# Performance work log

Hardware: AMD Instinct MI355X
Metric: run time of the kernel (lower is better)

## Reference

```python
import jax, jax.numpy as jnp
import numpy as np
import math

NV, NC, NE = 25000, 12500, 250000
DV_LP = DC_LP = 16
D_IN = 128   # in_var_dim = in_con_dim = in_edge_dim
D_OUT = 128  # out_var_dim = out_con_dim = out_edge_dim
E_WO = 5
EDGE_IN = D_IN + 3 + E_WO       # 136 = num_edge_lp_f_with_ss(8) + in_edge_dim(128)
VAR_COMB = DV_LP + D_IN          # 144
CON_COMB = DC_LP + D_IN          # 144

def _lin(key, din, dout, bias=True):
    k1, k2 = jax.random.split(key)
    W = jax.random.normal(k1, (din, dout), jnp.float32) * 0.05
    if bias:
        return W, jax.random.normal(k2, (dout,), jnp.float32) * 0.05
    return W, None

def setup_inputs():
    key = jax.random.key(0)
    ks = iter(jax.random.split(key, 64))
    d = {}
    d["var_learned_f"] = jax.random.normal(next(ks), (NV, D_IN), jnp.float32)
    d["var_lp_f"] = jax.random.normal(next(ks), (NV, DV_LP), jnp.float32)
    d["con_learned_f"] = jax.random.normal(next(ks), (NC, D_IN), jnp.float32)
    d["con_lp_f"] = jax.random.normal(next(ks), (NC, DC_LP), jnp.float32)
    d["edge_learned_f"] = jax.random.normal(next(ks), (NE, D_IN), jnp.float32)
    d["lo_costs"] = jax.random.normal(next(ks), (NE,), jnp.float32)
    d["hi_costs"] = jax.random.normal(next(ks), (NE,), jnp.float32)
    d["def_mm"] = jax.random.normal(next(ks), (NE,), jnp.float32)
    d["edge_lp_f_wo_ss"] = jax.random.normal(next(ks), (NE, E_WO), jnp.float32)
    # con_updater TransformerConv: src=var_comb(144), dst=con_comb(144), edge(136) -> 128
    d["cu_Wq"], d["cu_bq"] = _lin(next(ks), CON_COMB, D_OUT)
    d["cu_Wk"], d["cu_bk"] = _lin(next(ks), VAR_COMB, D_OUT)
    d["cu_Wv"], d["cu_bv"] = _lin(next(ks), VAR_COMB, D_OUT)
    d["cu_We"], _ = _lin(next(ks), EDGE_IN, D_OUT, bias=False)
    d["cu_Ws"], d["cu_bs"] = _lin(next(ks), CON_COMB, D_OUT)
    # var_updater TransformerConv: src=new con_comb(144), dst=var_comb(144)
    d["vu_Wq"], d["vu_bq"] = _lin(next(ks), VAR_COMB, D_OUT)
    d["vu_Wk"], d["vu_bk"] = _lin(next(ks), CON_COMB, D_OUT)
    d["vu_Wv"], d["vu_bv"] = _lin(next(ks), CON_COMB, D_OUT)
    d["vu_We"], _ = _lin(next(ks), EDGE_IN, D_OUT, bias=False)
    d["vu_Ws"], d["vu_bs"] = _lin(next(ks), VAR_COMB, D_OUT)
    # EdgeUpdater MLPs (hidden = out_edge_dim = 128, num_hidden_layers_edge = 0)
    d["eu_vW1"], d["eu_vb1"] = _lin(next(ks), VAR_COMB, D_OUT)
    d["eu_vW2"], d["eu_vb2"] = _lin(next(ks), D_OUT, D_OUT)
    d["eu_cW1"], d["eu_cb1"] = _lin(next(ks), CON_COMB, D_OUT)
    d["eu_cW2"], d["eu_cb2"] = _lin(next(ks), D_OUT, D_OUT)
    d["eu_eW1"], d["eu_eb1"] = _lin(next(ks), EDGE_IN + 2 * D_OUT, D_OUT)
    d["eu_eW2"], d["eu_eb2"] = _lin(next(ks), D_OUT, D_OUT)
    d["edge_index_var"] = jax.random.randint(next(ks), (NE,), 0, NV)
    d["edge_index_con"] = jax.random.randint(next(ks), (NE,), 0, NC)
    return d

def transformer_conv(x_src, x_dst, src_idx, dst_idx, e,
                     Wq, bq, Wk, bk, Wv, bv, We, Ws, bs, n_dst):
    # PyG TransformerConv, heads=1, edge_dim, aggr='mean', root_weight=True
    C = Wq.shape[1]
    q = x_dst @ Wq + bq                      # [N_dst, C]
    k = x_src @ Wk + bk                      # [N_src, C]
    v = x_src @ Wv + bv
    ee = e @ We                              # [E, C] (lin_edge, no bias)
    kj = k[src_idx] + ee
    alpha = jnp.sum(q[dst_idx] * kj, axis=-1) * (1.0 / math.sqrt(C))  # [E]
    # segment softmax over destination nodes
    amax = jax.ops.segment_max(alpha, dst_idx, num_segments=n_dst)
    ex = jnp.exp(alpha - amax[dst_idx])
    denom = jax.ops.segment_sum(ex, dst_idx, num_segments=n_dst)
    a = ex / denom[dst_idx]
    msg = (v[src_idx] + ee) * a[:, None]
    agg = jax.ops.segment_sum(msg, dst_idx, num_segments=n_dst)
    cnt = jax.ops.segment_sum(jnp.ones_like(alpha), dst_idx, num_segments=n_dst)
    out = agg / jnp.maximum(cnt, 1.0)[:, None]   # aggr='mean'
    return out + x_dst @ Ws + bs                 # skip connection (lin_skip)

def _forward(var_learned_f, var_lp_f, con_learned_f, con_lp_f, edge_learned_f,
             lo_costs, hi_costs, def_mm, edge_lp_f_wo_ss,
             cu_Wq, cu_bq, cu_Wk, cu_bk, cu_Wv, cu_bv, cu_We, cu_Ws, cu_bs,
             vu_Wq, vu_bq, vu_Wk, vu_bk, vu_Wv, vu_bv, vu_We, vu_Ws, vu_bs,
             eu_vW1, eu_vb1, eu_vW2, eu_vb2, eu_cW1, eu_cb1, eu_cW2, eu_cb2,
             eu_eW1, eu_eb1, eu_eW2, eu_eb2,
             edge_index_var, edge_index_con):
    relu = jax.nn.relu
    var_comb = jnp.concatenate([var_learned_f, var_lp_f], axis=1)     # [NV,144]
    con_comb = jnp.concatenate([con_learned_f, con_lp_f], axis=1)     # [NC,144]
    edge_comb = jnp.concatenate([edge_learned_f, lo_costs[:, None], hi_costs[:, None],
                                 def_mm[:, None], edge_lp_f_wo_ss], axis=1)  # [NE,136]
    # con update: messages from vars (edge_index[0]) to cons (edge_index[1])
    con_new = relu(transformer_conv(var_comb, con_comb, edge_index_var, edge_index_con,
                                    edge_comb, cu_Wq, cu_bq, cu_Wk, cu_bk, cu_Wv, cu_bv,
                                    cu_We, cu_Ws, cu_bs, NC))
    con_comb = jnp.concatenate([con_new, con_lp_f], axis=1)
    # var update: flow target_to_source -> messages from cons (edge_index[1]) to vars (edge_index[0])
    var_new = relu(transformer_conv(con_comb, var_comb, edge_index_con, edge_index_var,
                                    edge_comb, vu_Wq, vu_bq, vu_Wk, vu_bk, vu_Wv, vu_bv,
                                    vu_We, vu_Ws, vu_bs, NV))
    var_comb = jnp.concatenate([var_new, var_lp_f], axis=1)
    # edge update: compress nodes, gather to edges, concat, MLP
    vc = relu(relu(var_comb @ eu_vW1 + eu_vb1) @ eu_vW2 + eu_vb2)     # [NV,128]
    cc = relu(relu(con_comb @ eu_cW1 + eu_cb1) @ eu_cW2 + eu_cb2)     # [NC,128]
    h = jnp.concatenate([edge_comb, vc[edge_index_var], cc[edge_index_con]], axis=1)  # [NE,392]
    edge_new = relu(relu(h @ eu_eW1 + eu_eb1) @ eu_eW2 + eu_eb2)
    return var_new, con_new, edge_new

def reference(var_learned_f, var_lp_f, con_learned_f, con_lp_f, edge_learned_f,
              lo_costs, hi_costs, def_mm, edge_lp_f_wo_ss,
              cu_Wq, cu_bq, cu_Wk, cu_bk, cu_Wv, cu_bv, cu_We, cu_Ws, cu_bs,
              vu_Wq, vu_bq, vu_Wk, vu_bk, vu_Wv, vu_bv, vu_We, vu_Ws, vu_bs,
              eu_vW1, eu_vb1, eu_vW2, eu_vb2, eu_cW1, eu_cb1, eu_cW2, eu_cb2,
              eu_eW1, eu_eb1, eu_eW2, eu_eb2,
              edge_index_var, edge_index_con):
    return _forward(var_learned_f, var_lp_f, con_learned_f, con_lp_f, edge_learned_f,
                    lo_costs, hi_costs, def_mm, edge_lp_f_wo_ss,
                    cu_Wq, cu_bq, cu_Wk, cu_bk, cu_Wv, cu_bv, cu_We, cu_Ws, cu_bs,
                    vu_Wq, vu_bq, vu_Wk, vu_bk, vu_Wv, vu_bv, vu_We, vu_Ws, vu_bs,
                    eu_vW1, eu_vb1, eu_vW2, eu_vb2, eu_cW1, eu_cb1, eu_cW2, eu_cb2,
                    eu_eW1, eu_eb1, eu_eW2, eu_eb2,
                    edge_index_var, edge_index_con)
```

## Files before the change

kernel.cpp:

```cpp
#include <hip/hip_runtime.h>
#include <math.h>

#define NVV 25000
#define NCC 12500
#define NEE 250000
#define KP 160

typedef short bf16x8 __attribute__((ext_vector_type(8)));
typedef float f32x4 __attribute__((ext_vector_type(4)));

__device__ __forceinline__ unsigned short f2bf(float f) {
  unsigned u = __float_as_uint(f);
  u += 0x7fffu + ((u >> 16) & 1u);
  return (unsigned short)(u >> 16);
}
__device__ __forceinline__ float bf2f(unsigned short u) {
  return __uint_as_float((unsigned)u << 16);
}
__device__ __forceinline__ void gll16(const unsigned short* g, unsigned short* l) {
  __builtin_amdgcn_global_load_lds(
      (const __attribute__((address_space(1))) unsigned int*)(const void*)g,
      (__attribute__((address_space(3))) unsigned int*)(void*)l, 16, 0, 0);
}

__device__ __forceinline__ void stage_rows64(const unsigned short* __restrict__ X,
                                             unsigned short* As, int row0, int N,
                                             int wave, int lane) {
  #pragma unroll
  for (int j = 0; j < 5; ++j) {
    int inst = wave * 5 + j;
    int L = inst * 1024 + lane * 16;
    int kk = L >> 12;
    int r = (L >> 6) & 63;
    int ks = (L & 63) >> 1;
    int grow = row0 + r; if (grow >= N) grow = N - 1;
    gll16(X + (size_t)grow * KP + kk * 32 + ks, As + inst * 512);
  }
}

template <int MI, int NI>
__device__ __forceinline__ void zero_acc(f32x4 (&acc)[MI][NI]) {
  #pragma unroll
  for (int mi = 0; mi < MI; ++mi)
    #pragma unroll
    for (int ni = 0; ni < NI; ++ni) {
      acc[mi][ni][0] = 0.f; acc[mi][ni][1] = 0.f;
      acc[mi][ni][2] = 0.f; acc[mi][ni][3] = 0.f;
    }
}

template <int MI, int NI>
__device__ __forceinline__ void chunk_mfma_g(const unsigned short* As,
                                             const unsigned short* __restrict__ WT,
                                             f32x4 (&acc)[MI][NI], int kk,
                                             int wm, int wn, int fr, int fq) {
  bf16x8 av[MI], bv[NI];
  #pragma unroll
  for (int mi = 0; mi < MI; ++mi)
    av[mi] = *(const bf16x8*)&As[kk * 2048 + (wm + mi * 16 + fr) * 32 + fq * 8];
  #pragma unroll
  for (int ni = 0; ni < NI; ++ni)
    bv[ni] = *(const bf16x8*)&WT[(size_t)(wn + ni * 16 + fr) * KP + kk * 32 + fq * 8];
  #pragma unroll
  for (int mi = 0; mi < MI; ++mi)
    #pragma unroll
    for (int ni = 0; ni < NI; ++ni)
      acc[mi][ni] = __builtin_amdgcn_mfma_f32_16x16x32_bf16(av[mi], bv[ni],
                                                            acc[mi][ni], 0, 0, 0);
}

struct GJob {
  const unsigned short* X; const unsigned short* WT;
  const float* bias; const float* addf;
  float* outf; unsigned short* outb;
  int outb_stride, pad_flag, N, relu_flag;
};
struct GBatch { GJob j[4]; int start[4]; int njobs; };

__global__ __launch_bounds__(256, 8) void gemm_batch(GBatch B) {
  int job = 0;
  #pragma unroll
  for (int t = 1; t < 4; ++t)
    if (t < B.njobs && (int)blockIdx.x >= B.start[t]) job = t;
  GJob g = B.j[job];
  __shared__ unsigned short As[5 * 64 * 32];
  const int tid = threadIdx.x;
  const int lane = tid & 63, wave = tid >> 6;
  const int row0 = (blockIdx.x - B.start[job]) * 64;
  const int wm = (wave & 1) * 32, wn = (wave >> 1) * 64;
  const int fr = lane & 15, fq = lane >> 4;

  stage_rows64(g.X, As, row0, g.N, wave, lane);
  f32x4 acc[2][4];
  zero_acc<2, 4>(acc);
  __syncthreads();
  #pragma unroll
  for (int kk = 0; kk < 5; ++kk) chunk_mfma_g<2, 4>(As, g.WT, acc, kk, wm, wn, fr, fq);

  #pragma unroll
  for (int mi = 0; mi < 2; ++mi) {
    #pragma unroll
    for (int ni = 0; ni < 4; ++ni) {
      int gcol = wn + ni * 16 + fr;
      float bvv = g.bias ? g.bias[gcol] : 0.0f;
      #pragma unroll
      for (int r = 0; r < 4; ++r) {
        int grow = row0 + wm + mi * 16 + fq * 4 + r;
        if (grow < g.N) {
          float o = acc[mi][ni][r] + bvv;
          if (g.addf) o += g.addf[(size_t)grow * 128 + gcol];
          if (g.relu_flag) o = fmaxf(o, 0.f);
          if (g.outf) g.outf[(size_t)grow * 128 + gcol] = o;
          if (g.outb) g.outb[(size_t)grow * g.outb_stride + gcol] = f2bf(o);
        }
      }
    }
    if (g.outb && g.pad_flag && wn == 0) {
      #pragma unroll
      for (int r = 0; r < 4; ++r) {
        int grow = row0 + wm + mi * 16 + fq * 4 + r;
        if (grow < g.N)
          for (int pc = 128 + fr; pc < g.outb_stride; pc += 16)
            g.outb[(size_t)grow * g.outb_stride + pc] = 0;
      }
    }
  }
}

__global__ __launch_bounds__(256, 4) void gemm_t(
    const unsigned short* __restrict__ X, const unsigned short* __restrict__ WT,
    unsigned short* __restrict__ outb, int N) {
  __shared__ unsigned short As[5 * 64 * 32];
  const int tid = threadIdx.x;
  const int lane = tid & 63, wave = tid >> 6;
  const int row0 = blockIdx.x * 64;
  const int wm = (wave & 1) * 32, wn = (wave >> 1) * 80;
  const int fr = lane & 15, fq = lane >> 4;

  stage_rows64(X, As, row0, N, wave, lane);
  f32x4 acc[2][5];
  zero_acc<2, 5>(acc);
  __syncthreads();
  #pragma unroll
  for (int kk = 0; kk < 5; ++kk) chunk_mfma_g<2, 5>(As, WT, acc, kk, wm, wn, fr, fq);

  #pragma unroll
  for (int mi = 0; mi < 2; ++mi)
    #pragma unroll
    for (int ni = 0; ni < 5; ++ni) {
      int gcol = wn + ni * 16 + fr;
      #pragma unroll
      for (int r = 0; r < 4; ++r) {
        int grow = row0 + wm + mi * 16 + fq * 4 + r;
        if (grow < N) outb[(size_t)grow * KP + gcol] = f2bf(acc[mi][ni][r]);
      }
    }
}

__global__ __launch_bounds__(256, 4) void gemm_chain(
    const unsigned short* __restrict__ X,
    const unsigned short* __restrict__ W1, const float* __restrict__ b1,
    const unsigned short* __restrict__ gA, const unsigned short* __restrict__ gB,
    const int* __restrict__ giA, const int* __restrict__ giB,
    const unsigned short* __restrict__ W2, const float* __restrict__ b2,
    const unsigned short* __restrict__ W3, const float* __restrict__ b3,
    float* __restrict__ outf, unsigned short* __restrict__ outw,
    int N, int relu_last) {
  __shared__ unsigned short As[5 * 64 * 32];
  const int tid = threadIdx.x;
  const int lane = tid & 63, wave = tid >> 6;
  const int row0 = blockIdx.x * 64;
  const int wm = (wave & 1) * 32, wn = (wave >> 1) * 64;
  const int fr = lane & 15, fq = lane >> 4;

  stage_rows64(X, As, row0, N, wave, lane);
  f32x4 acc[2][4];
  zero_acc<2, 4>(acc);
  __syncthreads();
  #pragma unroll
  for (int kk = 0; kk < 5; ++kk) chunk_mfma_g<2, 4>(As, W1, acc, kk, wm, wn, fr, fq);

  __syncthreads();
  #pragma unroll
  for (int mi = 0; mi < 2; ++mi) {
    #pragma unroll
    for (int ni = 0; ni < 4; ++ni) {
      int col = wn + ni * 16 + fr;
      float bvv = b1 ? b1[col] : 0.0f;
      #pragma unroll
      for (int r = 0; r < 4; ++r) {
        int row = wm + mi * 16 + fq * 4 + r;
        int grow = row0 + row;
        int gi = (grow < N) ? grow : (N - 1);
        float o = acc[mi][ni][r] + bvv;
        if (gA) o += bf2f(gA[(size_t)giA[gi] * 128 + col]) +
                     bf2f(gB[(size_t)giB[gi] * 128 + col]);
        o = fmaxf(o, 0.f);
        As[(col >> 5) * 2048 + row * 32 + (col & 31)] = f2bf(o);
      }
    }
  }
  zero_acc<2, 4>(acc);
  __syncthreads();

  #pragma unroll
  for (int kk = 0; kk < 4; ++kk) chunk_mfma_g<2, 4>(As, W2, acc, kk, wm, wn, fr, fq);

  if (W3) {
    __syncthreads();
    #pragma unroll
    for (int mi = 0; mi < 2; ++mi) {
      #pragma unroll
      for (int ni = 0; ni < 4; ++ni) {
        int col = wn + ni * 16 + fr;
        float bvv = b2 ? b2[col] : 0.0f;
        #pragma unroll
        for (int r = 0; r < 4; ++r) {
          int row = wm + mi * 16 + fq * 4 + r;
          float o = fmaxf(acc[mi][ni][r] + bvv, 0.f);
          As[(col >> 5) * 2048 + row * 32 + (col & 31)] = f2bf(o);
        }
      }
    }
    zero_acc<2, 4>(acc);
    __syncthreads();
    #pragma unroll
    for (int kk = 0; kk < 4; ++kk) chunk_mfma_g<2, 4>(As, W3, acc, kk, wm, wn, fr, fq);
    #pragma unroll
    for (int mi = 0; mi < 2; ++mi)
      #pragma unroll
      for (int ni = 0; ni < 4; ++ni) {
        int gcol = wn + ni * 16 + fr;
        float bvv = b3 ? b3[gcol] : 0.0f;
        #pragma unroll
        for (int r = 0; r < 4; ++r) {
          int grow = row0 + wm + mi * 16 + fq * 4 + r;
          if (grow < N) {
            float o = acc[mi][ni][r] + bvv;
            if (relu_last) o = fmaxf(o, 0.f);
            if (outw) outw[(size_t)grow * 128 + gcol] = f2bf(o);
            else      outf[(size_t)grow * 128 + gcol] = o;
          }
        }
      }
  } else {
    #pragma unroll
    for (int mi = 0; mi < 2; ++mi)
      #pragma unroll
      for (int ni = 0; ni < 4; ++ni) {
        int gcol = wn + ni * 16 + fr;
        float bvv = b2 ? b2[gcol] : 0.0f;
        #pragma unroll
        for (int r = 0; r < 4; ++r) {
          int grow = row0 + wm + mi * 16 + fq * 4 + r;
          if (grow < N) {
            float o = acc[mi][ni][r] + bvv;
            if (relu_last) o = fmaxf(o, 0.f);
            if (outw) outw[(size_t)grow * 128 + gcol] = f2bf(o);
            else      outf[(size_t)grow * 128 + gcol] = o;
          }
        }
      }
  }
}

__global__ void build_node_bf(const float* __restrict__ learned, const float* __restrict__ lp,
                              unsigned short* __restrict__ out, int N) {
  int idx = blockIdx.x * blockDim.x + threadIdx.x;
  if (idx >= N * 40) return;
  int row = idx / 40, c4 = idx - row * 40;
  int c = c4 * 4;
  ushort4 o;
  if (c4 < 32) {
    const float* p = learned + (size_t)row * 128 + c;
    o.x = f2bf(p[0]); o.y = f2bf(p[1]); o.z = f2bf(p[2]); o.w = f2bf(p[3]);
  } else if (c4 < 36) {
    const float* p = lp + (size_t)row * 16 + (c - 128);
    o.x = f2bf(p[0]); o.y = f2bf(p[1]); o.z = f2bf(p[2]); o.w = f2bf(p[3]);
  } else { o.x = o.y = o.z = o.w = 0; }
  *(ushort4*)&out[(size_t)row * KP + c] = o;
}

__global__ void build_edge_bf(const float* __restrict__ el, const float* __restrict__ lo,
                              const float* __restrict__ hi, const float* __restrict__ dm,
                              const float* __restrict__ wo, unsigned short* __restrict__ out) {
  int idx = blockIdx.x * blockDim.x + threadIdx.x;
  if (idx >= NEE * 40) return;
  int row = idx / 40, c4 = idx - row * 40;
  int c = c4 * 4;
  ushort4 o;
  if (c4 < 32) {
    const float* p = el + (size_t)row * 128 + c;
    o.x = f2bf(p[0]); o.y = f2bf(p[1]); o.z = f2bf(p[2]); o.w = f2bf(p[3]);
  } else if (c4 == 32) {
    o.x = f2bf(lo[row]); o.y = f2bf(hi[row]); o.z = f2bf(dm[row]);
    o.w = f2bf(wo[(size_t)row * 5 + 0]);
  } else if (c4 == 33) {
    const float* p = wo + (size_t)row * 5;
    o.x = f2bf(p[1]); o.y = f2bf(p[2]); o.z = f2bf(p[3]); o.w = f2bf(p[4]);
  } else { o.x = o.y = o.z = o.w = 0; }
  *(ushort4*)&out[(size_t)row * KP + c] = o;
}

struct WJobs {
  const float* W[20];
  unsigned short* O[20];
  int K[20];
  int TR[20];
};
__global__ void convert_weights(WJobs j) {
  int b = blockIdx.x;
  int job = b / 100;
  int i = (b - job * 100) * 256 + threadIdx.x;
  int col = i / KP;
  int k = i - col * KP;
  float v = 0.f;
  if (j.TR[job]) { if (col < 128 && k < j.K[job]) v = j.W[job][(size_t)k * 128 + col]; }
  else           { if (col < 136 && k < j.K[job]) v = j.W[job][(size_t)col * 128 + k]; }
  j.O[job][(size_t)col * KP + k] = f2bf(v);
}

__global__ void zero2(int* __restrict__ a, int na, int* __restrict__ b, int nb) {
  int i = blockIdx.x * blockDim.x + threadIdx.x;
  if (i < na) a[i] = 0;
  if (i < nb) b[i] = 0;
}
__global__ void hist2(const int* __restrict__ dc, int* __restrict__ cc,
                      const int* __restrict__ dv, int* __restrict__ cv, int nE) {
  int e = blockIdx.x * blockDim.x + threadIdx.x;
  if (e >= nE) return;
  atomicAdd(&cc[dc[e]], 1);
  atomicAdd(&cv[dv[e]], 1);
}
__global__ void csr_scan(const int* __restrict__ counts, int* __restrict__ offsets,
                         int* __restrict__ cursor, int n) {
  __shared__ int part[256];
  int tid = threadIdx.x;
  int chunk = (n + 255) / 256;
  int lo = tid * chunk, hi = min(n, lo + chunk);
  int s = 0;
  for (int i = lo; i < hi; ++i) s += counts[i];
  part[tid] = s;
  __syncthreads();
  if (tid == 0) {
    int run = 0;
    for (int i = 0; i < 256; ++i) { int t = part[i]; part[i] = run; run += t; }
    offsets[n] = run;
  }
  __syncthreads();
  int base = part[tid];
  for (int i = lo; i < hi; ++i) { offsets[i] = base; cursor[i] = base; base += counts[i]; }
}
__global__ void csr_scatter(const int* __restrict__ dst, const int* __restrict__ src,
                            int* __restrict__ cursor, int* __restrict__ ce,
                            int* __restrict__ cs, int nE) {
  int e = blockIdx.x * blockDim.x + threadIdx.x;
  if (e >= nE) return;
  int pos = atomicAdd(&cursor[dst[e]], 1);
  ce[pos] = e;
  cs[pos] = src[e];
}

__global__ void fused_attn(
    const float* __restrict__ qbuf, const unsigned short* __restrict__ kbuf,
    const unsigned short* __restrict__ vbuf, const unsigned short* __restrict__ tbuf,
    const unsigned short* __restrict__ ecomb,
    const int* __restrict__ offsets, const int* __restrict__ ce,
    const int* __restrict__ cs, float* __restrict__ accVS,
    unsigned short* __restrict__ accE, int Nd) {
  int d = blockIdx.x * 4 + (threadIdx.x >> 6);
  if (d >= Nd) return;
  int lane = threadIdx.x & 63;
  int c = lane * 2;
  bool tl = (lane < 16);
  int c2 = 128 + c;
  float2 qv = *(const float2*)&qbuf[(size_t)d * 128 + c];
  unsigned tu = *(const unsigned*)&tbuf[(size_t)d * KP + c];
  float tx = __uint_as_float(tu << 16);
  float ty = __uint_as_float(tu & 0xffff0000u);
  float tx2 = 0.f, ty2 = 0.f;
  if (tl) {
    unsigned tu2 = *(const unsigned*)&tbuf[(size_t)d * KP + c2];
    tx2 = __uint_as_float(tu2 << 16);
    ty2 = __uint_as_float(tu2 & 0xffff0000u);
  }
  int beg = offsets[d], end = offsets[d + 1];
  float m = -INFINITY, l = 0.f;
  float ax = 0.f, ay = 0.f, axe = 0.f, aye = 0.f, axe2 = 0.f, aye2 = 0.f;
  const float SC = 0.08838834764831845f;
  int i = beg;
  for (; i + 1 < end; i += 2) {
    int ea = ce[i], sa = cs[i];
    int eb = ce[i + 1], sb = cs[i + 1];
    unsigned eua = *(const unsigned*)&ecomb[(size_t)ea * KP + c];
    unsigned eub = *(const unsigned*)&ecomb[(size_t)eb * KP + c];
    unsigned kua = *(const unsigned*)&kbuf[(size_t)sa * 128 + c];
    unsigned kub = *(const unsigned*)&kbuf[(size_t)sb * 128 + c];
    unsigned vua = *(const unsigned*)&vbuf[(size_t)sa * 128 + c];
    unsigned vub = *(const unsigned*)&vbuf[(size_t)sb * 128 + c];
    float a0 = __uint_as_float(eua << 16), a1 = __uint_as_float(eua & 0xffff0000u);
    float b0 = __uint_as_float(eub << 16), b1 = __uint_as_float(eub & 0xffff0000u);
    float a2 = 0.f, a3 = 0.f, b2 = 0.f, b3 = 0.f;
    if (tl) {
      unsigned eua2 = *(const unsigned*)&ecomb[(size_t)ea * KP + c2];
      unsigned eub2 = *(const unsigned*)&ecomb[(size_t)eb * KP + c2];
      a2 = __uint_as_float(eua2 << 16); a3 = __uint_as_float(eua2 & 0xffff0000u);
      b2 = __uint_as_float(eub2 << 16); b3 = __uint_as_float(eub2 & 0xffff0000u);
    }
    float pa = qv.x * __uint_as_float(kua << 16) + qv.y * __uint_as_float(kua & 0xffff0000u)
             + tx * a0 + ty * a1 + tx2 * a2 + ty2 * a3;
    float pb = qv.x * __uint_as_float(kub << 16) + qv.y * __uint_as_float(kub & 0xffff0000u)
             + tx * b0 + ty * b1 + tx2 * b2 + ty2 * b3;
    #pragma unroll
    for (int off = 1; off < 64; off <<= 1) {
      pa += __shfl_xor(pa, off, 64);
      pb += __shfl_xor(pb, off, 64);
    }
    {
      float alpha = pa * SC;
      float mn = fmaxf(m, alpha);
      float scale = __expf(m - mn);
      float w = __expf(alpha - mn);
      ax = ax * scale + __uint_as_float(vua << 16) * w;
      ay = ay * scale + __uint_as_float(vua & 0xffff0000u) * w;
      axe = axe * scale + a0 * w;   aye = aye * scale + a1 * w;
      axe2 = axe2 * scale + a2 * w; aye2 = aye2 * scale + a3 * w;
      l = l * scale + w; m = mn;
    }
    {
      float alpha = pb * SC;
      float mn = fmaxf(m, alpha);
      float scale = __expf(m - mn);
      float w = __expf(alpha - mn);
      ax = ax * scale + __uint_as_float(vub << 16) * w;
      ay = ay * scale + __uint_as_float(vub & 0xffff0000u) * w;
      axe = axe * scale + b0 * w;   aye = aye * scale + b1 * w;
      axe2 = axe2 * scale + b2 * w; aye2 = aye2 * scale + b3 * w;
      l = l * scale + w; m = mn;
    }
  }
  if (i < end) {
    int e = ce[i], s = cs[i];
    unsigned eu = *(const unsigned*)&ecomb[(size_t)e * KP + c];
    float e0 = __uint_as_float(eu << 16);
    float e1 = __uint_as_float(eu & 0xffff0000u);
    float e2 = 0.f, e3 = 0.f;
    if (tl) {
      unsigned eu2 = *(const unsigned*)&ecomb[(size_t)e * KP + c2];
      e2 = __uint_as_float(eu2 << 16);
      e3 = __uint_as_float(eu2 & 0xffff0000u);
    }
    unsigned ku = *(const unsigned*)&kbuf[(size_t)s * 128 + c];
    unsigned vu = *(const unsigned*)&vbuf[(size_t)s * 128 + c];
    float p = qv.x * __uint_as_float(ku << 16) + qv.y * __uint_as_float(ku & 0xffff0000u)
            + tx * e0 + ty * e1 + tx2 * e2 + ty2 * e3;
    #pragma unroll
    for (int off = 1; off < 64; off <<= 1) p += __shfl_xor(p, off, 64);
    float alpha = p * SC;
    float mn = fmaxf(m, alpha);
    float scale = __expf(m - mn);
    float w = __expf(alpha - mn);
    ax = ax * scale + __uint_as_float(vu << 16) * w;
    ay = ay * scale + __uint_as_float(vu & 0xffff0000u) * w;
    axe = axe * scale + e0 * w;   aye = aye * scale + e1 * w;
    axe2 = axe2 * scale + e2 * w; aye2 = aye2 * scale + e3 * w;
    l = l * scale + w; m = mn;
  }
  int deg = end - beg;
  float inv = (deg > 0) ? 1.0f / (l * (float)deg) : 0.0f;
  float2 sk = *(const float2*)&accVS[(size_t)d * 128 + c];
  *(float2*)&accVS[(size_t)d * 128 + c] = make_float2(ax * inv + sk.x, ay * inv + sk.y);
  ushort2 oe; oe.x = f2bf(axe * inv); oe.y = f2bf(aye * inv);
  *(ushort2*)&accE[(size_t)d * KP + c] = oe;
  if (tl) {
    ushort2 oe2; oe2.x = f2bf(axe2 * inv); oe2.y = f2bf(aye2 * inv);
    *(ushort2*)&accE[(size_t)d * KP + c2] = oe2;
  }
}

extern "C" void kernel_launch(void* const* d_in, const int* in_sizes, int n_in,
                              void* d_out, int out_size, void* d_ws, size_t ws_size,
                              hipStream_t stream) {
  const float* var_learned = (const float*)d_in[0];
  const float* var_lp      = (const float*)d_in[1];
  const float* con_learned = (const float*)d_in[2];
  const float* con_lp      = (const float*)d_in[3];
  const float* edge_learned= (const float*)d_in[4];
  const float* lo          = (const float*)d_in[5];
  const float* hi          = (const float*)d_in[6];
  const float* dm          = (const float*)d_in[7];
  const float* wo          = (const float*)d_in[8];
  const float* cu_Wq = (const float*)d_in[9],  *cu_bq = (const float*)d_in[10];
  const float* cu_Wk = (const float*)d_in[11], *cu_bk = (const float*)d_in[12];
  const float* cu_Wv = (const float*)d_in[13], *cu_bv = (const float*)d_in[14];
  const float* cu_We = (const float*)d_in[15];
  const float* cu_Ws = (const float*)d_in[16], *cu_bs = (const float*)d_in[17];
  const float* vu_Wq = (const float*)d_in[18], *vu_bq = (const float*)d_in[19];
  const float* vu_Wk = (const float*)d_in[20], *vu_bk = (const float*)d_in[21];
  const float* vu_Wv = (const float*)d_in[22], *vu_bv = (const float*)d_in[23];
  const float* vu_We = (const float*)d_in[24];
  const float* vu_Ws = (const float*)d_in[25], *vu_bs = (const float*)d_in[26];
  const float* eu_vW1 = (const float*)d_in[27], *eu_vb1 = (const float*)d_in[28];
  const float* eu_vW2 = (const float*)d_in[29], *eu_vb2 = (const float*)d_in[30];
  const float* eu_cW1 = (const float*)d_in[31], *eu_cb1 = (const float*)d_in[32];
  const float* eu_cW2 = (const float*)d_in[33], *eu_cb2 = (const float*)d_in[34];
  const float* eu_eW1 = (const float*)d_in[35], *eu_eb1 = (const float*)d_in[36];
  const float* eu_eW2 = (const float*)d_in[37], *eu_eb2 = (const float*)d_in[38];
  const int* eiv = (const int*)d_in[39];
  const int* eic = (const int*)d_in[40];

  float* out_var  = (float*)d_out;
  float* out_con  = out_var + (size_t)NVV * 128;
  float* out_edge = out_con + (size_t)NCC * 128;

  char* w = (char*)d_ws;
  auto alloc = [&](size_t bytes) { char* p = w; w += (bytes + 255) & ~(size_t)255; return p; };
  unsigned short* edge_comb_bf = (unsigned short*)alloc((size_t)NEE * KP * 2);
  unsigned short* var_comb_bf = (unsigned short*)alloc((size_t)NVV * KP * 2);
  unsigned short* con_comb_bf = (unsigned short*)alloc((size_t)NCC * KP * 2);
  unsigned short* q_bf    = (unsigned short*)alloc((size_t)NVV * KP * 2);
  unsigned short* t_bf    = (unsigned short*)alloc((size_t)NVV * KP * 2);
  unsigned short* accE_bf = (unsigned short*)alloc((size_t)NVV * KP * 2);
  unsigned short* kv_bf   = (unsigned short*)alloc((size_t)NVV * 128 * 2);
  unsigned short* vv_bf   = (unsigned short*)alloc((size_t)NVV * 128 * 2);
  unsigned short* vc_bf   = (unsigned short*)alloc((size_t)NVV * 128 * 2);
  unsigned short* cc_bf   = (unsigned short*)alloc((size_t)NCC * 128 * 2);
  float* bufV1 = (float*)alloc((size_t)NVV * 128 * 4);
  float* bufV2 = (float*)alloc((size_t)NVV * 128 * 4);
  float* bufC1 = (float*)alloc((size_t)NCC * 128 * 4);
  float* bufC2 = (float*)alloc((size_t)NCC * 128 * 4);
  unsigned short* WTbase = (unsigned short*)alloc((size_t)20 * 160 * KP * 2);
  int* countsC = (int*)alloc((size_t)NCC * 4);
  int* countsV = (int*)alloc((size_t)NVV * 4);
  int* offC = (int*)alloc((size_t)(NCC + 1) * 4);
  int* curC = (int*)alloc((size_t)NCC * 4);
  int* offV = (int*)alloc((size_t)(NVV + 1) * 4);
  int* curV = (int*)alloc((size_t)NVV * 4);
  int* ceA = (int*)alloc((size_t)NEE * 4);
  int* csA = (int*)alloc((size_t)NEE * 4);
  int* ceB = (int*)alloc((size_t)NEE * 4);
  int* csB = (int*)alloc((size_t)NEE * 4);
  (void)ws_size; (void)in_sizes; (void)n_in; (void)out_size;

  unsigned short* WT[20];
  for (int i = 0; i < 20; ++i) WT[i] = WTbase + (size_t)i * 160 * KP;
  WJobs jobs;
  const float* Wsrc[20] = {cu_Wq, cu_Wk, cu_Wv, cu_We, cu_Ws,
                           vu_Wq, vu_Wk, vu_Wv, vu_We, vu_Ws,
                           eu_vW1, eu_vW2, eu_cW1, eu_cW2,
                           eu_eW1, eu_eW1 + 136 * 128, eu_eW1 + 264 * 128, eu_eW2,
                           cu_We, vu_We};
  const int Ksrc[20] = {144, 144, 144, 136, 144, 144, 144, 144, 136, 144,
                        144, 128, 144, 128, 136, 128, 128, 128, 128, 128};
  const int Tsrc[20] = {1,1,1,1,1, 1,1,1,1,1, 1,1,1,1, 1,1,1,1, 0,0};
  for (int i = 0; i < 20; ++i) {
    jobs.W[i] = Wsrc[i]; jobs.O[i] = WT[i]; jobs.K[i] = Ksrc[i]; jobs.TR[i] = Tsrc[i];
  }

  const int T = 256;
  const int NBC = (NCC + 63) / 64;
  const int NBV = (NVV + 63) / 64;
  const int NBE = (NEE + 63) / 64;

  build_node_bf<<<(NVV * 40 + T - 1) / T, T, 0, stream>>>(var_learned, var_lp, var_comb_bf, NVV);
  build_node_bf<<<(NCC * 40 + T - 1) / T, T, 0, stream>>>(con_learned, con_lp, con_comb_bf, NCC);
  build_edge_bf<<<(NEE * 40 + T - 1) / T, T, 0, stream>>>(edge_learned, lo, hi, dm, wo, edge_comb_bf);
  convert_weights<<<20 * 100, T, 0, stream>>>(jobs);

  zero2<<<(NVV + T - 1) / T, T, 0, stream>>>(countsC, NCC, countsV, NVV);
  hist2<<<(NEE + T - 1) / T, T, 0, stream>>>(eic, countsC, eiv, countsV, NEE);
  csr_scan<<<1, 256, 0, stream>>>(countsC, offC, curC, NCC);
  csr_scan<<<1, 256, 0, stream>>>(countsV, offV, curV, NVV);
  csr_scatter<<<(NEE + T - 1) / T, T, 0, stream>>>(eic, eiv, curC, ceA, csA, NEE);
  csr_scatter<<<(NEE + T - 1) / T, T, 0, stream>>>(eiv, eic, curV, ceB, csB, NEE);

  {
    GBatch b{};
    b.j[0] = {con_comb_bf, WT[0], cu_bq, nullptr, bufC1, q_bf, KP, 1, NCC, 0};
    b.j[1] = {con_comb_bf, WT[4], cu_bs, nullptr, bufC2, nullptr, 0, 0, NCC, 0};
    b.j[2] = {var_comb_bf, WT[1], cu_bk, nullptr, nullptr, kv_bf, 128, 0, NVV, 0};
    b.j[3] = {var_comb_bf, WT[2], cu_bv, nullptr, nullptr, vv_bf, 128, 0, NVV, 0};
    b.start[0] = 0; b.start[1] = NBC; b.start[2] = 2 * NBC; b.start[3] = 2 * NBC + NBV;
    b.njobs = 4;
    gemm_batch<<<2 * NBC + 2 * NBV, 256, 0, stream>>>(b);
  }
  gemm_t<<<NBC, 256, 0, stream>>>(q_bf, WT[18], t_bf, NCC);
  fused_attn<<<(NCC + 3) / 4, 256, 0, stream>>>(bufC1, kv_bf, vv_bf, t_bf, edge_comb_bf,
                                                offC, ceA, csA, bufC2, accE_bf, NCC);
  {
    GBatch b{};
    b.j[0] = {accE_bf, WT[3], nullptr, bufC2, out_con, con_comb_bf, KP, 0, NCC, 1};
    b.start[0] = 0; b.njobs = 1;
    gemm_batch<<<NBC, 256, 0, stream>>>(b);
  }

  {
    GBatch b{};
    b.j[0] = {var_comb_bf, WT[5], vu_bq, nullptr, bufV1, q_bf, KP, 1, NVV, 0};
    b.j[1] = {var_comb_bf, WT[9], vu_bs, nullptr, bufV2, nullptr, 0, 0, NVV, 0};
    b.j[2] = {con_comb_bf, WT[6], vu_bk, nullptr, nullptr, kv_bf, 128, 0, NCC, 0};
    b.j[3] = {con_comb_bf, WT[7], vu_bv, nullptr, nullptr, vv_bf, 128, 0, NCC, 0};
    b.start[0] = 0; b.start[1] = NBV; b.start[2] = 2 * NBV; b.start[3] = 2 * NBV + NBC;
    b.njobs = 4;
    gemm_batch<<<2 * NBV + 2 * NBC, 256, 0, stream>>>(b);
  }
  gemm_t<<<NBV, 256, 0, stream>>>(q_bf, WT[19], t_bf, NVV);
  fused_attn<<<(NVV + 3) / 4, 256, 0, stream>>>(bufV1, kv_bf, vv_bf, t_bf, edge_comb_bf,
                                                offV, ceB, csB, bufV2, accE_bf, NVV);
  {
    GBatch b{};
    b.j[0] = {accE_bf, WT[8], nullptr, bufV2, out_var, var_comb_bf, KP, 0, NVV, 1};
    b.start[0] = 0; b.njobs = 1;
    gemm_batch<<<NBV, 256, 0, stream>>>(b);
  }

  gemm_chain<<<NBV, 256, 0, stream>>>(
      var_comb_bf, WT[10], eu_vb1, nullptr, nullptr, nullptr, nullptr,
      WT[11], eu_vb2, WT[15], nullptr, nullptr, vc_bf, NVV, 0);
  gemm_chain<<<NBC, 256, 0, stream>>>(
      con_comb_bf, WT[12], eu_cb1, nullptr, nullptr, nullptr, nullptr,
      WT[13], eu_cb2, WT[16], nullptr, nullptr, cc_bf, NCC, 0);
  gemm_chain<<<NBE, 256, 0, stream>>>(
      edge_comb_bf, WT[14], eu_eb1, vc_bf, cc_bf, eiv, eic,
      WT[17], eu_eb2, nullptr, nullptr, out_edge, nullptr, NEE, 1);
}
```

Measured before the change: 848.6 us.

## Pack CSR edge/source pairs, unroll attention gather by four, tune gemm_chain

CSR edge ids and source ids are packed into one int2 array, so the attention kernel does one 8-byte load per neighbor instead of two separate loads. The fused attention loop is unrolled from two to four neighbors to keep more gathers in flight, and the online-softmax update is factored into a helper. Separately, gemm_chain raises its launch-bounds occupancy hint from 4 to 8 and writes its fp32 output with nontemporal stores. The unroll and higher occupancy target may increase register pressure or force spills.

```diff
diff --git a/kernel.cpp b/kernel.cpp
--- a/kernel.cpp
+++ b/kernel.cpp
@@ -157,7 +157,7 @@
     }
 }
 
-__global__ __launch_bounds__(256, 4) void gemm_chain(
+__global__ __launch_bounds__(256, 8) void gemm_chain(
     const unsigned short* __restrict__ X,
     const unsigned short* __restrict__ W1, const float* __restrict__ b1,
     const unsigned short* __restrict__ gA, const unsigned short* __restrict__ gB,
@@ -239,7 +239,7 @@
             float o = acc[mi][ni][r] + bvv;
             if (relu_last) o = fmaxf(o, 0.f);
             if (outw) outw[(size_t)grow * 128 + gcol] = f2bf(o);
-            else      outf[(size_t)grow * 128 + gcol] = o;
+            else      __builtin_nontemporal_store(o, &outf[(size_t)grow * 128 + gcol]);
           }
         }
       }
@@ -257,7 +257,7 @@
             float o = acc[mi][ni][r] + bvv;
             if (relu_last) o = fmaxf(o, 0.f);
             if (outw) outw[(size_t)grow * 128 + gcol] = f2bf(o);
-            else      outf[(size_t)grow * 128 + gcol] = o;
+            else      __builtin_nontemporal_store(o, &outf[(size_t)grow * 128 + gcol]);
           }
         }
       }
@@ -352,22 +352,32 @@
   for (int i = lo; i < hi; ++i) { offsets[i] = base; cursor[i] = base; base += counts[i]; }
 }
 __global__ void csr_scatter(const int* __restrict__ dst, const int* __restrict__ src,
-                            int* __restrict__ cursor, int* __restrict__ ce,
-                            int* __restrict__ cs, int nE) {
+                            int* __restrict__ cursor, int2* __restrict__ ces, int nE) {
   int e = blockIdx.x * blockDim.x + threadIdx.x;
   if (e >= nE) return;
   int pos = atomicAdd(&cursor[dst[e]], 1);
-  ce[pos] = e;
-  cs[pos] = src[e];
+  ces[pos] = make_int2(e, src[e]);
+}
+
+struct AttSt { float m, l, ax, ay, axe, aye, axe2, aye2; };
+__device__ __forceinline__ void att_upd(AttSt& s, float alpha, unsigned vu,
+                                        float e0, float e1, float e2, float e3) {
+  float mn = fmaxf(s.m, alpha);
+  float scale = __expf(s.m - mn);
+  float w = __expf(alpha - mn);
+  s.ax = s.ax * scale + __uint_as_float(vu << 16) * w;
+  s.ay = s.ay * scale + __uint_as_float(vu & 0xffff0000u) * w;
+  s.axe = s.axe * scale + e0 * w;   s.aye = s.aye * scale + e1 * w;
+  s.axe2 = s.axe2 * scale + e2 * w; s.aye2 = s.aye2 * scale + e3 * w;
+  s.l = s.l * scale + w; s.m = mn;
 }
 
 __global__ void fused_attn(
     const float* __restrict__ qbuf, const unsigned short* __restrict__ kbuf,
     const unsigned short* __restrict__ vbuf, const unsigned short* __restrict__ tbuf,
     const unsigned short* __restrict__ ecomb,
-    const int* __restrict__ offsets, const int* __restrict__ ce,
-    const int* __restrict__ cs, float* __restrict__ accVS,
-    unsigned short* __restrict__ accE, int Nd) {
+    const int* __restrict__ offsets, const int2* __restrict__ ces,
+    float* __restrict__ accVS, unsigned short* __restrict__ accE, int Nd) {
   int d = blockIdx.x * 4 + (threadIdx.x >> 6);
   if (d >= Nd) return;
   int lane = threadIdx.x & 63;
@@ -385,95 +395,77 @@
     ty2 = __uint_as_float(tu2 & 0xffff0000u);
   }
   int beg = offsets[d], end = offsets[d + 1];
-  float m = -INFINITY, l = 0.f;
-  float ax = 0.f, ay = 0.f, axe = 0.f, aye = 0.f, axe2 = 0.f, aye2 = 0.f;
+  AttSt st{-INFINITY, 0.f, 0.f, 0.f, 0.f, 0.f, 0.f, 0.f};
   const float SC = 0.08838834764831845f;
   int i = beg;
-  for (; i + 1 < end; i += 2) {
-    int ea = ce[i], sa = cs[i];
-    int eb = ce[i + 1], sb = cs[i + 1];
-    unsigned eua = *(const unsigned*)&ecomb[(size_t)ea * KP + c];
-    unsigned eub = *(const unsigned*)&ecomb[(size_t)eb * KP + c];
-    unsigned kua = *(const unsigned*)&kbuf[(size_t)sa * 128 + c];
-    unsigned kub = *(const unsigned*)&kbuf[(size_t)sb * 128 + c];
-    unsigned vua = *(const unsigned*)&vbuf[(size_t)sa * 128 + c];
-    unsigned vub = *(const unsigned*)&vbuf[(size_t)sb * 128 + c];
-    float a0 = __uint_as_float(eua << 16), a1 = __uint_as_float(eua & 0xffff0000u);
-    float b0 = __uint_as_float(eub << 16), b1 = __uint_as_float(eub & 0xffff0000u);
-    float a2 = 0.f, a3 = 0.f, b2 = 0.f, b3 = 0.f;
+  for (; i + 3 < end; i += 4) {
+    int2 pr[4];
+    pr[0] = ces[i]; pr[1] = ces[i + 1]; pr[2] = ces[i + 2]; pr[3] = ces[i + 3];
+    unsigned eu[4], ku[4], vu[4];
+    float e0[4], e1[4], e2[4], e3[4], p[4];
+    #pragma unroll
+    for (int u = 0; u < 4; ++u) {
+      eu[u] = *(const unsigned*)&ecomb[(size_t)pr[u].x * KP + c];
+      ku[u] = *(const unsigned*)&kbuf[(size_t)pr[u].y * 128 + c];
+      vu[u] = *(const unsigned*)&vbuf[(size_t)pr[u].y * 128 + c];
+    }
+    #pragma unroll
+    for (int u = 0; u < 4; ++u) {
+      e0[u] = __uint_as_float(eu[u] << 16);
+      e1[u] = __uint_as_float(eu[u] & 0xffff0000u);
+      e2[u] = 0.f; e3[u] = 0.f;
+    }
     if (tl) {
-      unsigned eua2 = *(const unsigned*)&ecomb[(size_t)ea * KP + c2];
-      unsigned eub2 = *(const unsigned*)&ecomb[(size_t)eb * KP + c2];
-      a2 = __uint_as_float(eua2 << 16); a3 = __uint_as_float(eua2 & 0xffff0000u);
-      b2 = __uint_as_float(eub2 << 16); b3 = __uint_as_float(eub2 & 0xffff0000u);
-    }
-    float pa = qv.x * __uint_as_float(kua << 16) + qv.y * __uint_as_float(kua & 0xffff0000u)
-             + tx * a0 + ty * a1 + tx2 * a2 + ty2 * a3;
-    float pb = qv.x * __uint_as_float(kub << 16) + qv.y * __uint_as_float(kub & 0xffff0000u)
-             + tx * b0 + ty * b1 + tx2 * b2 + ty2 * b3;
+      #pragma unroll
+      for (int u = 0; u < 4; ++u) {
+        unsigned x = *(const unsigned*)&ecomb[(size_t)pr[u].x * KP + c2];
+        e2[u] = __uint_as_float(x << 16);
+        e3[u] = __uint_as_float(x & 0xffff0000u);
+      }
+    }
+    #pragma unroll
+    for (int u = 0; u < 4; ++u)
+      p[u] = qv.x * __uint_as_float(ku[u] << 16) + qv.y * __uint_as_float(ku[u] & 0xffff0000u)
+           + tx * e0[u] + ty * e1[u] + tx2 * e2[u] + ty2 * e3[u];
     #pragma unroll
     for (int off = 1; off < 64; off <<= 1) {
-      pa += __shfl_xor(pa, off, 64);
-      pb += __shfl_xor(pb, off, 64);
-    }
-    {
-      float alpha = pa * SC;
-      float mn = fmaxf(m, alpha);
-      float scale = __expf(m - mn);
-      float w = __expf(alpha - mn);
-      ax = ax * scale + __uint_as_float(vua << 16) * w;
-      ay = ay * scale + __uint_as_float(vua & 0xffff0000u) * w;
-      axe = axe * scale + a0 * w;   aye = aye * scale + a1 * w;
-      axe2 = axe2 * scale + a2 * w; aye2 = aye2 * scale + a3 * w;
-      l = l * scale + w; m = mn;
-    }
-    {
-      float alpha = pb * SC;
-      float mn = fmaxf(m, alpha);
-      float scale = __expf(m - mn);
-      float w = __expf(alpha - mn);
-      ax = ax * scale + __uint_as_float(vub << 16) * w;
-      ay = ay * scale + __uint_as_float(vub & 0xffff0000u) * w;
-      axe = axe * scale + b0 * w;   aye = aye * scale + b1 * w;
-      axe2 = axe2 * scale + b2 * w; aye2 = aye2 * scale + b3 * w;
-      l = l * scale + w; m = mn;
-    }
-  }
-  if (i < end) {
-    int e = ce[i], s = cs[i];
-    unsigned eu = *(const unsigned*)&ecomb[(size_t)e * KP + c];
+      p[0] += __shfl_xor(p[0], off, 64);
+      p[1] += __shfl_xor(p[1], off, 64);
+      p[2] += __shfl_xor(p[2], off, 64);
+      p[3] += __shfl_xor(p[3], off, 64);
+    }
+    #pragma unroll
+    for (int u = 0; u < 4; ++u)
+      att_upd(st, p[u] * SC, vu[u], e0[u], e1[u], e2[u], e3[u]);
+  }
+  for (; i < end; ++i) {
+    int2 pr = ces[i];
+    unsigned eu = *(const unsigned*)&ecomb[(size_t)pr.x * KP + c];
     float e0 = __uint_as_float(eu << 16);
     float e1 = __uint_as_float(eu & 0xffff0000u);
     float e2 = 0.f, e3 = 0.f;
     if (tl) {
-      unsigned eu2 = *(const unsigned*)&ecomb[(size_t)e * KP + c2];
-      e2 = __uint_as_float(eu2 << 16);
-      e3 = __uint_as_float(eu2 & 0xffff0000u);
-    }
-    unsigned ku = *(const unsigned*)&kbuf[(size_t)s * 128 + c];
-    unsigned vu = *(const unsigned*)&vbuf[(size_t)s * 128 + c];
+      unsigned x = *(const unsigned*)&ecomb[(size_t)pr.x * KP + c2];
+      e2 = __uint_as_float(x << 16);
+      e3 = __uint_as_float(x & 0xffff0000u);
+    }
+    unsigned ku = *(const unsigned*)&kbuf[(size_t)pr.y * 128 + c];
+    unsigned vu = *(const unsigned*)&vbuf[(size_t)pr.y * 128 + c];
     float p = qv.x * __uint_as_float(ku << 16) + qv.y * __uint_as_float(ku & 0xffff0000u)
             + tx * e0 + ty * e1 + tx2 * e2 + ty2 * e3;
     #pragma unroll
     for (int off = 1; off < 64; off <<= 1) p += __shfl_xor(p, off, 64);
-    float alpha = p * SC;
-    float mn = fmaxf(m, alpha);
-    float scale = __expf(m - mn);
-    float w = __expf(alpha - mn);
-    ax = ax * scale + __uint_as_float(vu << 16) * w;
-    ay = ay * scale + __uint_as_float(vu & 0xffff0000u) * w;
-    axe = axe * scale + e0 * w;   aye = aye * scale + e1 * w;
-    axe2 = axe2 * scale + e2 * w; aye2 = aye2 * scale + e3 * w;
-    l = l * scale + w; m = mn;
+    att_upd(st, p * SC, vu, e0, e1, e2, e3);
   }
   int deg = end - beg;
-  float inv = (deg > 0) ? 1.0f / (l * (float)deg) : 0.0f;
+  float inv = (deg > 0) ? 1.0f / (st.l * (float)deg) : 0.0f;
   float2 sk = *(const float2*)&accVS[(size_t)d * 128 + c];
-  *(float2*)&accVS[(size_t)d * 128 + c] = make_float2(ax * inv + sk.x, ay * inv + sk.y);
-  ushort2 oe; oe.x = f2bf(axe * inv); oe.y = f2bf(aye * inv);
+  *(float2*)&accVS[(size_t)d * 128 + c] =
+      make_float2(st.ax * inv + sk.x, st.ay * inv + sk.y);
+  ushort2 oe; oe.x = f2bf(st.axe * inv); oe.y = f2bf(st.aye * inv);
   *(ushort2*)&accE[(size_t)d * KP + c] = oe;
   if (tl) {
-    ushort2 oe2; oe2.x = f2bf(axe2 * inv); oe2.y = f2bf(aye2 * inv);
+    ushort2 oe2; oe2.x = f2bf(st.axe2 * inv); oe2.y = f2bf(st.aye2 * inv);
     *(ushort2*)&accE[(size_t)d * KP + c2] = oe2;
   }
 }
@@ -536,10 +528,8 @@
   int* curC = (int*)alloc((size_t)NCC * 4);
   int* offV = (int*)alloc((size_t)(NVV + 1) * 4);
   int* curV = (int*)alloc((size_t)NVV * 4);
-  int* ceA = (int*)alloc((size_t)NEE * 4);
-  int* csA = (int*)alloc((size_t)NEE * 4);
-  int* ceB = (int*)alloc((size_t)NEE * 4);
-  int* csB = (int*)alloc((size_t)NEE * 4);
+  int2* cesA = (int2*)alloc((size_t)NEE * 8);
+  int2* cesB = (int2*)alloc((size_t)NEE * 8);
   (void)ws_size; (void)in_sizes; (void)n_in; (void)out_size;
 
   unsigned short* WT[20];
@@ -571,8 +561,8 @@
   hist2<<<(NEE + T - 1) / T, T, 0, stream>>>(eic, countsC, eiv, countsV, NEE);
   csr_scan<<<1, 256, 0, stream>>>(countsC, offC, curC, NCC);
   csr_scan<<<1, 256, 0, stream>>>(countsV, offV, curV, NVV);
-  csr_scatter<<<(NEE + T - 1) / T, T, 0, stream>>>(eic, eiv, curC, ceA, csA, NEE);
-  csr_scatter<<<(NEE + T - 1) / T, T, 0, stream>>>(eiv, eic, curV, ceB, csB, NEE);
+  csr_scatter<<<(NEE + T - 1) / T, T, 0, stream>>>(eic, eiv, curC, cesA, NEE);
+  csr_scatter<<<(NEE + T - 1) / T, T, 0, stream>>>(eiv, eic, curV, cesB, NEE);
 
   {
     GBatch b{};
@@ -586,7 +576,7 @@
   }
   gemm_t<<<NBC, 256, 0, stream>>>(q_bf, WT[18], t_bf, NCC);
   fused_attn<<<(NCC + 3) / 4, 256, 0, stream>>>(bufC1, kv_bf, vv_bf, t_bf, edge_comb_bf,
-                                                offC, ceA, csA, bufC2, accE_bf, NCC);
+                                                offC, cesA, bufC2, accE_bf, NCC);
   {
     GBatch b{};
     b.j[0] = {accE_bf, WT[3], nullptr, bufC2, out_con, con_comb_bf, KP, 0, NCC, 1};
@@ -606,7 +596,7 @@
   }
   gemm_t<<<NBV, 256, 0, stream>>>(q_bf, WT[19], t_bf, NVV);
   fused_attn<<<(NVV + 3) / 4, 256, 0, stream>>>(bufV1, kv_bf, vv_bf, t_bf, edge_comb_bf,
-                                                offV, ceB, csB, bufV2, accE_bf, NVV);
+                                                offV, cesB, bufV2, accE_bf, NVV);
   {
     GBatch b{};
     b.j[0] = {accE_bf, WT[8], nullptr, bufV2, out_var, var_comb_bf, KP, 0, NVV, 1};
```

Result: slower. 940.4 us (+10.8%).
